# Kernel tuning notes

Measured on AMD Instinct MI355X. Metric: run time of the kernel, lower is better.

Reference implementation:

```python
import jax, jax.numpy as jnp
import numpy as np

R = 32           # voxel resolution
NEG_SLOPE = 0.1  # LeakyReLU slope in PVCNN voxel layers
BN_EPS = 1e-4    # BatchNorm3d eps used by PVCNN


def _voxelize(features, coords):
    # features [B,C,N], coords [B,3,N]; normalize=True, eps=0
    B, C, N = features.shape
    norm = coords - coords.mean(axis=2, keepdims=True)
    scale = jnp.linalg.norm(norm, axis=1).max(axis=1)        # [B] max point radius
    norm = norm / (scale[:, None, None] * 2.0) + 0.5         # -> roughly [0,1]
    norm = jnp.clip(norm * R, 0.0, R - 1)                    # float coords in [0,R-1]
    v = jnp.round(norm).astype(jnp.int32)                    # [B,3,N]
    idx = (v[:, 0] * R + v[:, 1]) * R + v[:, 2]              # [B,N] flat voxel index

    def scatter_avg(f, i):  # f [C,N], i [N]
        cnt = jnp.zeros((R ** 3,), f.dtype).at[i].add(1.0)
        s = jnp.zeros((f.shape[0], R ** 3), f.dtype).at[:, i].add(f)
        return s / jnp.maximum(cnt, 1.0)

    grid = jax.vmap(scatter_avg)(features, idx).reshape(B, C, R, R, R)
    return grid, norm


def _devoxelize(grid, coords):
    # grid [B,C,R,R,R], coords float [B,3,N] in [0, R-1]
    B, C = grid.shape[:2]
    flat = grid.reshape(B, C, R ** 3)
    lo = jnp.floor(coords).astype(jnp.int32)
    f = coords - lo
    hi = jnp.minimum(lo + 1, R - 1)
    x0, y0, z0 = lo[:, 0], lo[:, 1], lo[:, 2]
    x1, y1, z1 = hi[:, 0], hi[:, 1], hi[:, 2]
    fx, fy, fz = f[:, 0], f[:, 1], f[:, 2]

    def corner(ix, iy, iz, w):
        idx = (ix * R + iy) * R + iz                          # [B,N]
        g = jax.vmap(lambda gf, ii: gf[:, ii])(flat, idx)     # [B,C,N]
        return g * w[:, None, :]

    return (corner(x0, y0, z0, (1 - fx) * (1 - fy) * (1 - fz))
            + corner(x0, y0, z1, (1 - fx) * (1 - fy) * fz)
            + corner(x0, y1, z0, (1 - fx) * fy * (1 - fz))
            + corner(x0, y1, z1, (1 - fx) * fy * fz)
            + corner(x1, y0, z0, fx * (1 - fy) * (1 - fz))
            + corner(x1, y0, z1, fx * (1 - fy) * fz)
            + corner(x1, y1, z0, fx * fy * (1 - fz))
            + corner(x1, y1, z1, fx * fy * fz))


def _conv_bn_lrelu(x, w, b, gamma, beta, mean, var):
    y = jax.lax.conv_general_dilated(
        x, w, window_strides=(1, 1, 1), padding='SAME',
        dimension_numbers=('NCDHW', 'OIDHW', 'NCDHW'))
    y = y + b[None, :, None, None, None]
    scale = gamma / jnp.sqrt(var + BN_EPS)
    y = (y - mean[None, :, None, None, None]) * scale[None, :, None, None, None] \
        + beta[None, :, None, None, None]
    return jnp.where(y >= 0, y, NEG_SLOPE * y)


def setup_inputs() -> dict:
    key = jax.random.key(0)
    ks = jax.random.split(key, 16)
    B, C, N = 8, 64, 65536
    inp = {
        'features': jax.random.normal(ks[0], (B, C, N), jnp.float32),
        'coords': jax.random.normal(ks[1], (B, 3, N), jnp.float32),
        'w1': jax.random.normal(ks[2], (64, 64, 3, 3, 3), jnp.float32) * 0.05,
        'b1': jax.random.normal(ks[3], (64,), jnp.float32) * 0.05,
        'g1': jax.random.uniform(ks[4], (64,), jnp.float32) + 0.5,
        'be1': jax.random.normal(ks[5], (64,), jnp.float32) * 0.1,
        'm1': jax.random.normal(ks[6], (64,), jnp.float32) * 0.1,
        'v1': jax.random.uniform(ks[7], (64,), jnp.float32) + 0.5,
        'w2': jax.random.normal(ks[8], (64, 64, 3, 3, 3), jnp.float32) * 0.05,
        'b2': jax.random.normal(ks[9], (64,), jnp.float32) * 0.05,
        'g2': jax.random.uniform(ks[10], (64,), jnp.float32) + 0.5,
        'be2': jax.random.normal(ks[11], (64,), jnp.float32) * 0.1,
        'm2': jax.random.normal(ks[12], (64,), jnp.float32) * 0.1,
        'v2': jax.random.uniform(ks[13], (64,), jnp.float32) + 0.5,
    }
    return inp


def reference(features, coords, w1, b1, g1, be1, m1, v1,
              w2, b2, g2, be2, m2, v2):
    grid, vox_coords = _voxelize(features, coords)           # [B,C,R,R,R], [B,3,N]
    grid = _conv_bn_lrelu(grid, w1, b1, g1, be1, m1, v1)
    grid = _conv_bn_lrelu(grid, w2, b2, g2, be2, m2, v2)
    point_feats = _devoxelize(grid, vox_coords)              # [B,Cout,N]
    return (point_feats, coords)
```

## Files before the change

kernel.cpp:

```cpp
#include <hip/hip_runtime.h>
#include <hip/hip_bf16.h>
#include <hip/hip_fp16.h>

#define NPTS   65536
#define BATCH  8
#define CH     64
#define RES    32
#define RCELLS 32768
#define NEG_SLOPE 0.1f
#define BN_EPS 1e-4f
#define GSPLIT 4

typedef float    f32x4 __attribute__((ext_vector_type(4)));
typedef _Float16 f16x8 __attribute__((ext_vector_type(8)));
typedef _Float16 f16x4 __attribute__((ext_vector_type(4)));

#define OFF_SUMS   0
#define OFF_SCALE  24
#define OFF_CNT    32
#define OFF_IDX    (OFF_CNT + BATCH*RCELLS)
#define OFF_CSTART (OFF_IDX + BATCH*NPTS)
#define OFF_ORDER  (OFF_CSTART + BATCH*RCELLS)
#define OFF_BN     (OFF_ORDER + BATCH*NPTS)
#define OFF_WP1    (OFF_BN + 256)
#define OFF_WP2    (OFF_WP1 + 55296)
#define OFF_FT     (OFF_WP2 + 55296)
#define OFF_GA     (OFF_FT + 16777216)
#define OFF_GB     (OFF_GA + 8388608)

__device__ inline float waveReduceSum(float v) {
#pragma unroll
    for (int off = 32; off > 0; off >>= 1) v += __shfl_down(v, off, 64);
    return v;
}
__device__ inline float waveReduceMax(float v) {
#pragma unroll
    for (int off = 32; off > 0; off >>= 1) v = fmaxf(v, __shfl_down(v, off, 64));
    return v;
}

__global__ __launch_bounds__(256) void k_stats_sum(const float* __restrict__ coords,
                                                   float* __restrict__ sums) {
    __shared__ float sm[3][4];
    int b = blockIdx.x >> 3, chunk = blockIdx.x & 7;
    const float* cb = coords + (size_t)b * 3 * NPTS;
    float s0 = 0.f, s1 = 0.f, s2 = 0.f;
    for (int i = threadIdx.x; i < 8192; i += 256) {
        int n = chunk * 8192 + i;
        s0 += cb[n];
        s1 += cb[n + NPTS];
        s2 += cb[n + 2 * NPTS];
    }
    s0 = waveReduceSum(s0); s1 = waveReduceSum(s1); s2 = waveReduceSum(s2);
    int lane = threadIdx.x & 63, wid = threadIdx.x >> 6;
    if (lane == 0) { sm[0][wid] = s0; sm[1][wid] = s1; sm[2][wid] = s2; }
    __syncthreads();
    if (threadIdx.x == 0) {
        atomicAdd(&sums[b * 3 + 0], sm[0][0] + sm[0][1] + sm[0][2] + sm[0][3]);
        atomicAdd(&sums[b * 3 + 1], sm[1][0] + sm[1][1] + sm[1][2] + sm[1][3]);
        atomicAdd(&sums[b * 3 + 2], sm[2][0] + sm[2][1] + sm[2][2] + sm[2][3]);
    }
}

__global__ __launch_bounds__(256) void k_stats_max(const float* __restrict__ coords,
                                                   const float* __restrict__ sums,
                                                   unsigned int* __restrict__ scaleBits) {
    __shared__ float sm[4];
    int b = blockIdx.x >> 3, chunk = blockIdx.x & 7;
    const float* cb = coords + (size_t)b * 3 * NPTS;
    float mx = sums[b * 3 + 0] * (1.f / NPTS);
    float my = sums[b * 3 + 1] * (1.f / NPTS);
    float mz = sums[b * 3 + 2] * (1.f / NPTS);
    float m = 0.f;
    for (int i = threadIdx.x; i < 8192; i += 256) {
        int n = chunk * 8192 + i;
        float dx = cb[n] - mx, dy = cb[n + NPTS] - my, dz = cb[n + 2 * NPTS] - mz;
        m = fmaxf(m, sqrtf(dx * dx + dy * dy + dz * dz));
    }
    m = waveReduceMax(m);
    int lane = threadIdx.x & 63, wid = threadIdx.x >> 6;
    if (lane == 0) sm[wid] = m;
    __syncthreads();
    if (threadIdx.x == 0) {
        float r = fmaxf(fmaxf(sm[0], sm[1]), fmaxf(sm[2], sm[3]));
        atomicMax(&scaleBits[b], __float_as_uint(r));
    }
}

__global__ __launch_bounds__(256) void k_vox_assign(const float* __restrict__ coords,
                                                    const float* __restrict__ sums,
                                                    const unsigned int* __restrict__ scaleBits,
                                                    int* __restrict__ idxb,
                                                    int* __restrict__ cnt) {
    int g = blockIdx.x * 256 + threadIdx.x;
    int b = g >> 16, n = g & (NPTS - 1);
    const float* cb = coords + (size_t)b * 3 * NPTS;
    float scale2 = __uint_as_float(scaleBits[b]) * 2.f;
    int v[3];
#pragma unroll
    for (int d = 0; d < 3; ++d) {
        float mean = sums[b * 3 + d] * (1.f / NPTS);
        float x = (cb[d * NPTS + n] - mean) / scale2 + 0.5f;
        x *= (float)RES;
        x = fminf(fmaxf(x, 0.f), (float)(RES - 1));
        v[d] = (int)rintf(x);
    }
    int id = (v[0] * RES + v[1]) * RES + v[2];
    idxb[b * NPTS + n] = id;
    atomicAdd(&cnt[b * RCELLS + id], 1);
}

__global__ __launch_bounds__(256) void k_scan(const int* __restrict__ cnt,
                                              int* __restrict__ cellStart) {
    __shared__ int bufA[256], bufB[256];
    int b = blockIdx.x, tid = threadIdx.x;
    const int* cb = cnt + b * RCELLS;
    int sum = 0;
    for (int i = 0; i < 128; ++i) sum += cb[tid * 128 + i];
    bufA[tid] = sum;
    __syncthreads();
    int* src = bufA; int* dst = bufB;
    for (int off = 1; off < 256; off <<= 1) {
        int v = src[tid];
        if (tid >= off) v += src[tid - off];
        dst[tid] = v;
        __syncthreads();
        int* t = src; src = dst; dst = t;
    }
    int run = (tid > 0) ? src[tid - 1] : 0;
    int* cs = cellStart + b * RCELLS;
    for (int i = 0; i < 128; ++i) {
        int c = cb[tid * 128 + i];
        cs[tid * 128 + i] = run;
        run += c;
    }
}

__global__ __launch_bounds__(256) void k_rank(const int* __restrict__ idxb,
                                              int* __restrict__ cellStart,
                                              int* __restrict__ order) {
    int g = blockIdx.x * 256 + threadIdx.x;
    int b = g >> 16, n = g & (NPTS - 1);
    int cell = idxb[b * NPTS + n];
    int pos = atomicAdd(&cellStart[b * RCELLS + cell], 1);
    order[b * NPTS + pos] = n;
}

__global__ __launch_bounds__(256) void k_transpose(const float* __restrict__ f,
                                                   _Float16* __restrict__ featT) {
    int g = blockIdx.x * 256 + threadIdx.x;
    int b = g >> 16, n = g & (NPTS - 1);
    const float* fb = f + (size_t)b * CH * NPTS + n;
    _Float16* dst = featT + (size_t)g * 64;
#pragma unroll
    for (int k = 0; k < 8; ++k) {
        f16x8 hv;
#pragma unroll
        for (int j = 0; j < 8; ++j)
            hv[j] = (_Float16)fb[(size_t)(k * 8 + j) * NPTS];
        *(f16x8*)(dst + k * 8) = hv;
    }
}

__global__ __launch_bounds__(256) void k_gather(const _Float16* __restrict__ featT,
                                                const int* __restrict__ order,
                                                const int* __restrict__ cellStart,
                                                const int* __restrict__ cnt,
                                                _Float16* __restrict__ gA) {
    int bi = blockIdx.x;
    int b  = bi & 7;
    int chunk = bi >> 3;
    int r  = chunk * 256 + threadIdx.x;
    int sub  = r & (GSPLIT - 1);
    int ct   = (r >> 2) & 1;
    int cell = r >> 3;

    int e0 = cellStart[b * RCELLS + cell];
    int c  = cnt[b * RCELLS + cell];
    int s0 = e0 - c;
    int len = (c + GSPLIT - 1) >> 2;
    int s = s0 + sub * len;
    int e = min(s + len, e0);

    float acc[32];
#pragma unroll
    for (int j = 0; j < 32; ++j) acc[j] = 0.f;
    const int* ob = order + b * NPTS;
    const _Float16* fb = featT + (((size_t)b << 16)) * 64 + ct * 32;

    int p = s;
    for (; p + 8 <= e; p += 8) {
        int n[8];
#pragma unroll
        for (int u = 0; u < 8; ++u) n[u] = ob[p + u];
        f16x8 v[8][4];
#pragma unroll
        for (int u = 0; u < 8; ++u) {
            const _Float16* q = fb + (size_t)n[u] * 64;
#pragma unroll
            for (int k = 0; k < 4; ++k)
                v[u][k] = *(const f16x8*)(q + k * 8);
        }
#pragma unroll
        for (int u = 0; u < 8; ++u)
#pragma unroll
            for (int k = 0; k < 4; ++k)
#pragma unroll
                for (int j = 0; j < 8; ++j)
                    acc[k * 8 + j] += (float)v[u][k][j];
    }
    for (; p < e; ++p) {
        int n = ob[p];
        const _Float16* q = fb + (size_t)n * 64;
#pragma unroll
        for (int k = 0; k < 4; ++k) {
            f16x8 vv = *(const f16x8*)(q + k * 8);
#pragma unroll
            for (int j = 0; j < 8; ++j)
                acc[k * 8 + j] += (float)vv[j];
        }
    }

#pragma unroll
    for (int j = 0; j < 32; ++j) {
        acc[j] += __shfl_xor(acc[j], 1, 64);
        acc[j] += __shfl_xor(acc[j], 2, 64);
    }

    if (sub == 0) {
        float inv = 1.f / (float)max(c, 1);
        _Float16* dst = gA + ((size_t)(b * 2 + ct) * RCELLS + cell) * 32;
#pragma unroll
        for (int k = 0; k < 4; ++k) {
            f16x8 hv;
#pragma unroll
            for (int j = 0; j < 8; ++j)
                hv[j] = (_Float16)(acc[k * 8 + j] * inv);
            *(f16x8*)(dst + k * 8) = hv;
        }
    }
}

__global__ __launch_bounds__(256) void k_prep(const float* __restrict__ w,
                                              const float* __restrict__ bias,
                                              const float* __restrict__ g,
                                              const float* __restrict__ be,
                                              const float* __restrict__ m,
                                              const float* __restrict__ v,
                                              _Float16* __restrict__ wP,
                                              float* __restrict__ bnA,
                                              float* __restrict__ bnB) {
    int s = blockIdx.x * 256 + threadIdx.x;
    int ci_in = s & 31;
    int t  = s >> 5;
    int co = t & 63;
    int tc = t >> 6;
    int ct = tc & 1;
    int tap = tc >> 1;
    int ci = ct * 32 + ci_in;
    wP[s] = (_Float16)w[co * 1728 + ci * 27 + tap];
    if (s < 64) {
        float A = g[s] / sqrtf(v[s] + BN_EPS);
        bnA[s] = A;
        bnB[s] = (bias[s] - m[s]) * A + be[s];
    }
}

__global__ __launch_bounds__(256, 2) void k_conv(const _Float16* __restrict__ gIn,
                                                 _Float16* __restrict__ gOut,
                                                 const _Float16* __restrict__ wP,
                                                 const float* __restrict__ bnA,
                                                 const float* __restrict__ bnB) {
    __shared__ _Float16 sIn[3 * 10 * 34 * 32];
    int bi = blockIdx.x;
    int b  = bi >> 7;
    int rem = bi & 127;
    int z  = rem >> 2;
    int yg = rem & 3;
    int tid = threadIdx.x;
    int wid = tid >> 6;
    int lane = tid & 63;
    int l15 = lane & 15, quad = lane >> 4;

    f32x4 acc[4][4];
#pragma unroll
    for (int mt = 0; mt < 4; ++mt)
#pragma unroll
        for (int nt = 0; nt < 4; ++nt) acc[mt][nt] = (f32x4){0.f, 0.f, 0.f, 0.f};

    const f16x8* wp8 = (const f16x8*)wP;

    int bbase[4];
#pragma unroll
    for (int nt = 0; nt < 4; ++nt) {
        int yl = 2 * wid + (nt >> 1);
        int x  = ((nt & 1) << 4) + l15;
        bbase[nt] = ((10 + (yl + 1)) * 34 + (x + 1)) * 32 + quad * 8;
    }

    for (int ct = 0; ct < 2; ++ct) {
        const _Float16* gin = gIn + (size_t)(b * 2 + ct) * (RCELLS * 32);
#pragma unroll
        for (int it = 0; it < 16; ++it) {
            int s = tid + it * 256;
            if (s < 4080) {
                int cc  = s & 3;
                int pos = s >> 2;
                int xx  = pos % 34;
                int t2  = pos / 34;
                int yy  = t2 % 10;
                int zz  = t2 / 10;
                int x = xx - 1, y = yg * 8 + yy - 1, z0 = z + zz - 1;
                f32x4 val = {0.f, 0.f, 0.f, 0.f};
                if ((unsigned)x < 32u && (unsigned)y < 32u && (unsigned)z0 < 32u)
                    val = *(const f32x4*)(gin + ((size_t)((z0 * 32 + y) * 32 + x)) * 32 + cc * 8);
                *(f32x4*)(sIn + (size_t)s * 8) = val;
            }
        }
        __syncthreads();

#pragma unroll
        for (int dz = -1; dz <= 1; ++dz)
#pragma unroll
        for (int dy = -1; dy <= 1; ++dy)
#pragma unroll
        for (int dx = -1; dx <= 1; ++dx) {
            int tap = (dz + 1) * 9 + (dy + 1) * 3 + (dx + 1);
            f16x8 aF[4];
#pragma unroll
            for (int mt = 0; mt < 4; ++mt)
                aF[mt] = wp8[tap * 512 + ct * 256 + mt * 64 + l15 * 4 + quad];
            f16x8 bF[4];
            int off = ((dz + 1) * 340 + dy * 34 + dx) * 32 - 340 * 32;
#pragma unroll
            for (int nt = 0; nt < 4; ++nt)
                bF[nt] = *(const f16x8*)(sIn + bbase[nt] + off);
#pragma unroll
            for (int mt = 0; mt < 4; ++mt)
#pragma unroll
                for (int nt = 0; nt < 4; ++nt)
                    acc[mt][nt] = __builtin_amdgcn_mfma_f32_16x16x32_f16(
                        aF[mt], bF[nt], acc[mt][nt], 0, 0, 0);
        }
        __syncthreads();
    }

#pragma unroll
    for (int nt = 0; nt < 4; ++nt) {
        int y = yg * 8 + 2 * wid + (nt >> 1);
        int x = ((nt & 1) << 4) + l15;
        int cell = z * 1024 + y * 32 + x;
#pragma unroll
        for (int mt = 0; mt < 4; ++mt) {
            int cob = mt * 16 + quad * 4;
            f32x4 An = *(const f32x4*)(bnA + cob);
            f32x4 Bn = *(const f32x4*)(bnB + cob);
            f16x4 hv;
#pragma unroll
            for (int r = 0; r < 4; ++r) {
                float t = acc[mt][nt][r] * An[r] + Bn[r];
                t = (t >= 0.f) ? t : NEG_SLOPE * t;
                hv[r] = (_Float16)t;
            }
            _Float16* op = gOut + ((size_t)(b * 2 + (cob >> 5)) * RCELLS + cell) * 32 + (cob & 31);
            *(f16x4*)op = hv;
        }
    }
}

__global__ __launch_bounds__(256) void k_devox(const _Float16* __restrict__ gA,
                                               const float* __restrict__ coords,
                                               const float* __restrict__ sums,
                                               const unsigned int* __restrict__ scaleBits,
                                               float* __restrict__ out) {
    int g = blockIdx.x * 256 + threadIdx.x;
    int b = g >> 17;
    int ct = (g >> 16) & 1;
    int n = g & (NPTS - 1);
    const float* cb = coords + (size_t)b * 3 * NPTS;
    float scale2 = __uint_as_float(scaleBits[b]) * 2.f;
    float nc[3];
#pragma unroll
    for (int d = 0; d < 3; ++d) {
        float mean = sums[b * 3 + d] * (1.f / NPTS);
        float x = (cb[d * NPTS + n] - mean) / scale2 + 0.5f;
        x *= (float)RES;
        nc[d] = fminf(fmaxf(x, 0.f), (float)(RES - 1));
    }
    float tx = nc[0], ty = nc[1], tz = nc[2];
    float lx = floorf(tx), ly = floorf(ty), lz = floorf(tz);
    float fx = tx - lx, fy = ty - ly, fz = tz - lz;
    int x0 = (int)lx, y0 = (int)ly, z0 = (int)lz;
    int x1 = min(x0 + 1, RES - 1), y1 = min(y0 + 1, RES - 1), z1 = min(z0 + 1, RES - 1);
    int ids[8];
    float wc[8];
    ids[0] = (x0 * RES + y0) * RES + z0;
    ids[1] = (x0 * RES + y0) * RES + z1;
    ids[2] = (x0 * RES + y1) * RES + z0;
    ids[3] = (x0 * RES + y1) * RES + z1;
    ids[4] = (x1 * RES + y0) * RES + z0;
    ids[5] = (x1 * RES + y0) * RES + z1;
    ids[6] = (x1 * RES + y1) * RES + z0;
    ids[7] = (x1 * RES + y1) * RES + z1;
    float gx = 1.f - fx, gy = 1.f - fy, gz = 1.f - fz;
    wc[0] = gx * gy * gz; wc[1] = gx * gy * fz;
    wc[2] = gx * fy * gz; wc[3] = gx * fy * fz;
    wc[4] = fx * gy * gz; wc[5] = fx * gy * fz;
    wc[6] = fx * fy * gz; wc[7] = fx * fy * fz;

    float acc[32];
#pragma unroll
    for (int j = 0; j < 32; ++j) acc[j] = 0.f;
    const _Float16* gb = gA + (size_t)(b * 2 + ct) * RCELLS * 32;
#pragma unroll
    for (int c8 = 0; c8 < 8; ++c8) {
        const _Float16* p = gb + (size_t)ids[c8] * 32;
        float wgt = wc[c8];
#pragma unroll
        for (int k = 0; k < 4; ++k) {
            f16x8 v = *(const f16x8*)(p + k * 8);
#pragma unroll
            for (int j = 0; j < 8; ++j)
                acc[k * 8 + j] += wgt * (float)v[j];
        }
    }
    float* ob = out + (size_t)b * CH * NPTS + (size_t)(ct * 32) * NPTS + n;
#pragma unroll
    for (int j = 0; j < 32; ++j)
        __builtin_nontemporal_store(acc[j], ob + (size_t)j * NPTS);
}

extern "C" void kernel_launch(void* const* d_in, const int* in_sizes, int n_in,
                              void* d_out, int out_size, void* d_ws, size_t ws_size,
                              hipStream_t stream) {
    const float* features = (const float*)d_in[0];
    const float* coords   = (const float*)d_in[1];
    const float* w1  = (const float*)d_in[2];
    const float* b1  = (const float*)d_in[3];
    const float* g1  = (const float*)d_in[4];
    const float* be1 = (const float*)d_in[5];
    const float* m1  = (const float*)d_in[6];
    const float* v1  = (const float*)d_in[7];
    const float* w2  = (const float*)d_in[8];
    const float* b2  = (const float*)d_in[9];
    const float* g2  = (const float*)d_in[10];
    const float* be2 = (const float*)d_in[11];
    const float* m2  = (const float*)d_in[12];
    const float* v2  = (const float*)d_in[13];

    float* ws = (float*)d_ws;
    float*        sums      = ws + OFF_SUMS;
    unsigned int* scaleBits = (unsigned int*)(ws + OFF_SCALE);
    int*          cnt       = (int*)(ws + OFF_CNT);
    int*          idxb      = (int*)(ws + OFF_IDX);
    int*          cellStart = (int*)(ws + OFF_CSTART);
    int*          order     = (int*)(ws + OFF_ORDER);
    float*        bnA1      = ws + OFF_BN;
    float*        bnB1      = ws + OFF_BN + 64;
    float*        bnA2      = ws + OFF_BN + 128;
    float*        bnB2      = ws + OFF_BN + 192;
    _Float16*     wP1       = (_Float16*)(ws + OFF_WP1);
    _Float16*     wP2       = (_Float16*)(ws + OFF_WP2);
    _Float16*     featT     = (_Float16*)(ws + OFF_FT);
    _Float16*     gA        = (_Float16*)(ws + OFF_GA);
    _Float16*     gB        = (_Float16*)(ws + OFF_GB);

    (void)hipMemsetAsync(ws, 0, (size_t)(OFF_IDX) * sizeof(float), stream);

    k_stats_sum<<<64, 256, 0, stream>>>(coords, sums);
    k_stats_max<<<64, 256, 0, stream>>>(coords, sums, scaleBits);
    k_vox_assign<<<(BATCH * NPTS) / 256, 256, 0, stream>>>(coords, sums, scaleBits,
                                                           idxb, cnt);
    k_scan<<<BATCH, 256, 0, stream>>>(cnt, cellStart);
    k_rank<<<(BATCH * NPTS) / 256, 256, 0, stream>>>(idxb, cellStart, order);
    k_transpose<<<(BATCH * NPTS) / 256, 256, 0, stream>>>(features, featT);
    k_gather<<<(BATCH * RCELLS * 2 * GSPLIT) / 256, 256, 0, stream>>>(
        featT, order, cellStart, cnt, gA);
    k_prep<<<432, 256, 0, stream>>>(w1, b1, g1, be1, m1, v1, wP1, bnA1, bnB1);
    k_prep<<<432, 256, 0, stream>>>(w2, b2, g2, be2, m2, v2, wP2, bnA2, bnB2);
    k_conv<<<BATCH * RES * 4, 256, 0, stream>>>(gA, gB, wP1, bnA1, bnB1);
    k_conv<<<BATCH * RES * 4, 256, 0, stream>>>(gB, gA, wP2, bnA2, bnB2);
    k_devox<<<(2 * BATCH * NPTS) / 256, 256, 0, stream>>>(gA, coords, sums, scaleBits,
                                                          (float*)d_out);

    (void)hipMemcpyAsync((float*)d_out + (size_t)BATCH * CH * NPTS, coords,
                         (size_t)BATCH * 3 * NPTS * sizeof(float),
                         hipMemcpyDeviceToDevice, stream);
}
```

Before: 718.2 us.

## Split devoxelize into coord prep pass and 4-lanes-per-point gather kernel

```diff
diff --git a/kernel.cpp b/kernel.cpp
--- a/kernel.cpp
+++ b/kernel.cpp
@@ -27,6 +27,7 @@
 #define OFF_FT     (OFF_WP2 + 55296)
 #define OFF_GA     (OFF_FT + 16777216)
 #define OFF_GB     (OFF_GA + 8388608)
+#define OFF_META   OFF_FT
 
 __device__ inline float waveReduceSum(float v) {
 #pragma unroll
@@ -368,15 +369,12 @@
     }
 }
 
-__global__ __launch_bounds__(256) void k_devox(const _Float16* __restrict__ gA,
-                                               const float* __restrict__ coords,
+__global__ __launch_bounds__(256) void k_dprep(const float* __restrict__ coords,
                                                const float* __restrict__ sums,
                                                const unsigned int* __restrict__ scaleBits,
-                                               float* __restrict__ out) {
+                                               f32x4* __restrict__ meta) {
     int g = blockIdx.x * 256 + threadIdx.x;
-    int b = g >> 17;
-    int ct = (g >> 16) & 1;
-    int n = g & (NPTS - 1);
+    int b = g >> 16, n = g & (NPTS - 1);
     const float* cb = coords + (size_t)b * 3 * NPTS;
     float scale2 = __uint_as_float(scaleBits[b]) * 2.f;
     float nc[3];
@@ -387,46 +385,60 @@
         x *= (float)RES;
         nc[d] = fminf(fmaxf(x, 0.f), (float)(RES - 1));
     }
-    float tx = nc[0], ty = nc[1], tz = nc[2];
-    float lx = floorf(tx), ly = floorf(ty), lz = floorf(tz);
-    float fx = tx - lx, fy = ty - ly, fz = tz - lz;
+    float lx = floorf(nc[0]), ly = floorf(nc[1]), lz = floorf(nc[2]);
     int x0 = (int)lx, y0 = (int)ly, z0 = (int)lz;
-    int x1 = min(x0 + 1, RES - 1), y1 = min(y0 + 1, RES - 1), z1 = min(z0 + 1, RES - 1);
-    int ids[8];
-    float wc[8];
-    ids[0] = (x0 * RES + y0) * RES + z0;
-    ids[1] = (x0 * RES + y0) * RES + z1;
-    ids[2] = (x0 * RES + y1) * RES + z0;
-    ids[3] = (x0 * RES + y1) * RES + z1;
-    ids[4] = (x1 * RES + y0) * RES + z0;
-    ids[5] = (x1 * RES + y0) * RES + z1;
-    ids[6] = (x1 * RES + y1) * RES + z0;
-    ids[7] = (x1 * RES + y1) * RES + z1;
+    int dx = (x0 + 1 <= RES - 1) ? 1 : 0;
+    int dy = (y0 + 1 <= RES - 1) ? 1 : 0;
+    int dz = (z0 + 1 <= RES - 1) ? 1 : 0;
+    int id0 = (x0 * RES + y0) * RES + z0;
+    int pk = id0 | (dx << 15) | (dy << 16) | (dz << 17);
+    f32x4 m;
+    m[0] = nc[0] - lx; m[1] = nc[1] - ly; m[2] = nc[2] - lz;
+    m[3] = __int_as_float(pk);
+    meta[(size_t)b * NPTS + n] = m;
+}
+
+__global__ __launch_bounds__(256) void k_devox(const _Float16* __restrict__ gA,
+                                               const f32x4* __restrict__ meta,
+                                               float* __restrict__ out) {
+    int w = blockIdx.x * 4 + (threadIdx.x >> 6);
+    int lane = threadIdx.x & 63;
+    int psub = lane & 15;
+    int chunk = lane >> 4;
+    int ct = w & 1;
+    int group = w >> 1;
+    int b = group >> 12;
+    int n0 = (group & 4095) << 4;
+    int n = n0 + psub;
+
+    f32x4 m = meta[(size_t)b * NPTS + n];
+    float fx = m[0], fy = m[1], fz = m[2];
+    int pk = __float_as_int(m[3]);
+    int id0 = pk & 32767;
+    int xo = ((pk >> 15) & 1) << 10;
+    int yo = ((pk >> 16) & 1) << 5;
+    int zo = (pk >> 17) & 1;
     float gx = 1.f - fx, gy = 1.f - fy, gz = 1.f - fz;
-    wc[0] = gx * gy * gz; wc[1] = gx * gy * fz;
-    wc[2] = gx * fy * gz; wc[3] = gx * fy * fz;
-    wc[4] = fx * gy * gz; wc[5] = fx * gy * fz;
-    wc[6] = fx * fy * gz; wc[7] = fx * fy * fz;
-
-    float acc[32];
-#pragma unroll
-    for (int j = 0; j < 32; ++j) acc[j] = 0.f;
-    const _Float16* gb = gA + (size_t)(b * 2 + ct) * RCELLS * 32;
-#pragma unroll
-    for (int c8 = 0; c8 < 8; ++c8) {
-        const _Float16* p = gb + (size_t)ids[c8] * 32;
-        float wgt = wc[c8];
-#pragma unroll
-        for (int k = 0; k < 4; ++k) {
-            f16x8 v = *(const f16x8*)(p + k * 8);
-#pragma unroll
-            for (int j = 0; j < 8; ++j)
-                acc[k * 8 + j] += wgt * (float)v[j];
-        }
-    }
-    float* ob = out + (size_t)b * CH * NPTS + (size_t)(ct * 32) * NPTS + n;
-#pragma unroll
-    for (int j = 0; j < 32; ++j)
+
+    const _Float16* gb = gA + (size_t)(b * 2 + ct) * (RCELLS * 32) + chunk * 8;
+
+    float acc[8];
+#pragma unroll
+    for (int j = 0; j < 8; ++j) acc[j] = 0.f;
+
+#pragma unroll
+    for (int c = 0; c < 8; ++c) {
+        int id = id0 + ((c & 4) ? xo : 0) + ((c & 2) ? yo : 0) + ((c & 1) ? zo : 0);
+        float wgt = ((c & 4) ? fx : gx) * ((c & 2) ? fy : gy) * ((c & 1) ? fz : gz);
+        f16x8 v = *(const f16x8*)(gb + (size_t)id * 32);
+#pragma unroll
+        for (int j = 0; j < 8; ++j)
+            acc[j] += wgt * (float)v[j];
+    }
+
+    float* ob = out + (size_t)b * CH * NPTS + (size_t)(ct * 32 + chunk * 8) * NPTS + n;
+#pragma unroll
+    for (int j = 0; j < 8; ++j)
         __builtin_nontemporal_store(acc[j], ob + (size_t)j * NPTS);
 }
 
@@ -462,6 +474,7 @@
     _Float16*     wP1       = (_Float16*)(ws + OFF_WP1);
     _Float16*     wP2       = (_Float16*)(ws + OFF_WP2);
     _Float16*     featT     = (_Float16*)(ws + OFF_FT);
+    f32x4*        meta      = (f32x4*)(ws + OFF_META);
     _Float16*     gA        = (_Float16*)(ws + OFF_GA);
     _Float16*     gB        = (_Float16*)(ws + OFF_GB);
 
@@ -479,9 +492,9 @@
     k_prep<<<432, 256, 0, stream>>>(w1, b1, g1, be1, m1, v1, wP1, bnA1, bnB1);
     k_prep<<<432, 256, 0, stream>>>(w2, b2, g2, be2, m2, v2, wP2, bnA2, bnB2);
     k_conv<<<BATCH * RES * 4, 256, 0, stream>>>(gA, gB, wP1, bnA1, bnB1);
+    k_dprep<<<(BATCH * NPTS) / 256, 256, 0, stream>>>(coords, sums, scaleBits, meta);
     k_conv<<<BATCH * RES * 4, 256, 0, stream>>>(gB, gA, wP2, bnA2, bnB2);
-    k_devox<<<(2 * BATCH * NPTS) / 256, 256, 0, stream>>>(gA, coords, sums, scaleBits,
-                                                          (float*)d_out);
+    k_devox<<<(2 * BATCH * NPTS / 16) / 4, 256, 0, stream>>>(gA, meta, (float*)d_out);
 
     (void)hipMemcpyAsync((float*)d_out + (size_t)BATCH * CH * NPTS, coords,
                          (size_t)BATCH * 3 * NPTS * sizeof(float),
```

Result: faster. 692.7 us (-3.5%).
